# Kernel optimization log

Hardware: AMD Instinct MI355X
Metric: run time of the kernel (lower is better)

Reference implementation:

```python
import jax, jax.numpy as jnp
import numpy as np

B, S1, S2, S3 = 2, 64, 64, 40
INIT_STEP, NUM_CH = 10, 1
WIDTH, MODES, TMODES = 64, 12, 8
GRID_DIM = 3
N_LAYERS = 4


def setup_inputs() -> dict:
    key = jax.random.key(0)
    ks = jax.random.split(key, 16)
    scale = 1.0 / (WIDTH * WIDTH)
    d_in = INIT_STEP * NUM_CH + GRID_DIM
    return {
        "x": jax.random.normal(ks[0], (B, S1, S2, S3, INIT_STEP * NUM_CH), jnp.float32),
        "p_w": jax.random.normal(ks[1], (WIDTH, d_in), jnp.float32) * 0.05,
        "p_b": jnp.zeros((WIDTH,), jnp.float32),
        # radial spectral weights (reflection=False): lower-center column + lower-right block, stacked over 4 layers
        "W_LC": scale * jax.random.uniform(ks[2], (N_LAYERS, WIDTH, WIDTH, MODES, 1, TMODES), jnp.float32),
        "W_LR": scale * jax.random.uniform(ks[3], (N_LAYERS, WIDTH, WIDTH, MODES - 1, MODES - 1, TMODES), jnp.float32),
        "mlp_w1": jax.random.normal(ks[4], (N_LAYERS, WIDTH, WIDTH), jnp.float32) * 0.05,
        "mlp_b1": jnp.zeros((N_LAYERS, WIDTH), jnp.float32),
        "mlp_w2": jax.random.normal(ks[5], (N_LAYERS, WIDTH, WIDTH), jnp.float32) * 0.05,
        "mlp_b2": jnp.zeros((N_LAYERS, WIDTH), jnp.float32),
        "w_w": jax.random.normal(ks[6], (N_LAYERS, WIDTH, WIDTH), jnp.float32) * 0.05,
        "w_b": jnp.zeros((N_LAYERS, WIDTH), jnp.float32),
        "q_w1": jax.random.normal(ks[7], (4 * WIDTH, WIDTH), jnp.float32) * 0.05,
        "q_b1": jnp.zeros((4 * WIDTH,), jnp.float32),
        "q_w2": jax.random.normal(ks[8], (NUM_CH, 4 * WIDTH), jnp.float32) * 0.05,
        "q_b2": jnp.zeros((NUM_CH,), jnp.float32),
    }


def _add_grid(x):
    b, s1, s2, s3, _ = x.shape
    gx = jnp.linspace(0.0, 1.0, s1, dtype=x.dtype)
    gy = jnp.linspace(0.0, 1.0, s2, dtype=x.dtype)
    gt = jnp.linspace(0.0, 1.0, s3, dtype=x.dtype)
    g = jnp.stack(jnp.meshgrid(gx, gy, gt, indexing="ij"), axis=-1)  # (s1,s2,s3,3)
    g = jnp.broadcast_to(g[None], (b, s1, s2, s3, GRID_DIM))
    return jnp.concatenate([x, g], axis=-1)


def _rot90(a):
    # torch.rot90(a, k=1, dims=[-3,-2]) == transpose(flip(a, -2), (-3,-2))
    return jnp.swapaxes(jnp.flip(a, axis=-2), -3, -2)


def _spectral_weights(W_LC, W_LR):
    # W_LC: (i,o,m,1,tm), W_LR: (i,o,m-1,m-1,tm) -> full radial weight (i,o,2m-1,2m-1,tm)
    W_LRf = jnp.concatenate([W_LC[:, :, 1:], W_LR], axis=-2)                    # (i,o,m-1,m,tm)
    W_UR = jnp.concatenate([jnp.flip(W_LC, axis=-3), _rot90(W_LRf)], axis=-2)   # (i,o,m,m,tm)
    W_R = jnp.concatenate([W_UR, W_LRf], axis=-3)                               # (i,o,2m-1,m,tm)
    return jnp.concatenate([jnp.flip(W_R[..., 1:, :], axis=(-3, -2)), W_R], axis=-2)


def _spectral_conv(x, W_LC, W_LR):
    b, ci, s1, s2, s3 = x.shape
    f0y, f0x = s1 // 2, s2 // 2  # index of zero freq after fftshift
    W = _spectral_weights(W_LC, W_LR)
    x_ft = jnp.fft.fftshift(jnp.fft.rfftn(x, axes=(-3, -2, -1)), axes=(-3, -2))
    xs = x_ft[..., f0y - MODES + 1:f0y + MODES, f0x - MODES + 1:f0x + MODES, :TMODES]
    out = jnp.einsum("bixyz,ioxyz->boxyz", xs, W.astype(xs.dtype))
    co = W.shape[1]
    out_ft = jnp.zeros((b, co, s1, s2, s3 // 2 + 1), dtype=xs.dtype)
    out_ft = out_ft.at[..., f0y - MODES + 1:f0y + MODES, f0x - MODES + 1:f0x + MODES, :TMODES].set(out)
    return jnp.fft.irfftn(jnp.fft.ifftshift(out_ft, axes=(-3, -2)), s=(s1, s2, s3), axes=(-3, -2, -1))


def _conv1x1(x, w, b):
    return jnp.einsum("bixyz,oi->boxyz", x, w) + b[None, :, None, None, None]


def _mlp3d(x, w1, b1, w2, b2):
    h = jax.nn.gelu(_conv1x1(x, w1, b1), approximate=False)
    return _conv1x1(h, w2, b2)


def _forward(x, p_w, p_b, W_LC, W_LR, mlp_w1, mlp_b1, mlp_w2, mlp_b2, w_w, w_b, q_w1, q_b1, q_w2, q_b2):
    x = _add_grid(x)
    x = jnp.einsum("bxyzi,wi->bxyzw", x, p_w) + p_b
    x = jnp.transpose(x, (0, 4, 1, 2, 3))  # (B, width, S1, S2, S3)
    for l in range(N_LAYERS):
        x1 = _spectral_conv(x, W_LC[l], W_LR[l])
        x1 = _mlp3d(x1, mlp_w1[l], mlp_b1[l], mlp_w2[l], mlp_b2[l])
        x2 = _conv1x1(x, w_w[l], w_b[l])
        x = x1 + x2
        if l < N_LAYERS - 1:
            x = jax.nn.relu(x)
    x = _mlp3d(x, q_w1, q_b1, q_w2, q_b2)
    return jnp.transpose(x, (0, 2, 3, 4, 1))


def reference(x, p_w, p_b, W_LC, W_LR, mlp_w1, mlp_b1, mlp_w2, mlp_b2, w_w, w_b, q_w1, q_b1, q_w2, q_b2):
    return _forward(x, p_w, p_b, W_LC, W_LR, mlp_w1, mlp_b1, mlp_w2, mlp_b2, w_w, w_b, q_w1, q_b1, q_w2, q_b2)
```

## Files before the change

kernel.cpp:

```cpp
#include <hip/hip_runtime.h>
#include <math.h>

#define PI_D 3.14159265358979323846

__global__ void k_tables(float* tzf, float* tzi, float* tz2, float* tzk,
                         float* txf, float* txi) {
    int t = blockIdx.x * blockDim.x + threadIdx.x;
    if (t < 320) {
        int z = t >> 3, k = t & 7;
        double ang = -2.0 * PI_D * (double)(z * k) / 40.0;
        tzf[t * 2] = (float)cos(ang); tzf[t * 2 + 1] = (float)sin(ang);
        tzi[t * 2] = (float)cos(-ang); tzi[t * 2 + 1] = (float)sin(-ang);
        double s = 1.0 / 163840.0;
        double f = (k == 0) ? s : 2.0 * s;
        tz2[t * 2] = (float)(f * cos(-ang));
        tz2[t * 2 + 1] = (k == 0) ? 0.0f : (float)(-f * sin(-ang));
        tzk[(k * 40 + z) * 2] = (float)cos(ang);
        tzk[(k * 40 + z) * 2 + 1] = (float)sin(ang);
    }
    if (t < 1472) {
        int xx = t / 23, m = t % 23;
        double ang = -2.0 * PI_D * (double)(xx * (m - 11)) / 64.0;
        txf[t * 2] = (float)cos(ang); txf[t * 2 + 1] = (float)sin(ang);
        txi[t * 2] = (float)cos(-ang); txi[t * 2 + 1] = (float)sin(-ang);
    }
}

__global__ void k_wtrans(const float* __restrict__ w2, const float* __restrict__ ww,
                         const float* __restrict__ w1,
                         float* __restrict__ w2t, float* __restrict__ wwt,
                         float* __restrict__ w1t) {
    int gid = blockIdx.x * blockDim.x + threadIdx.x;
    if (gid < 16384) {
        int l = gid >> 12, r = gid & 4095, o = r >> 6, i = r & 63;
        w2t[l * 4096 + i * 64 + o] = w2[l * 4096 + o * 64 + i];
        wwt[l * 4096 + i * 64 + o] = ww[l * 4096 + o * 64 + i];
        w1t[l * 4096 + i * 64 + o] = w1[l * 4096 + o * 64 + i];
    }
}

__global__ void k_lift(const float* __restrict__ xin, const float* __restrict__ pw,
                       const float* __restrict__ pb, float* __restrict__ xo) {
    int gid = blockIdx.x * 256 + threadIdx.x;
    int b = gid / 163840, p = gid % 163840;
    int y = p / 2560, xx = (p / 40) % 64, z = p % 40;
    float v[13];
#pragma unroll
    for (int i = 0; i < 10; i++) v[i] = xin[(size_t)gid * 10 + i];
    v[10] = (float)((double)y / 63.0);
    v[11] = (float)((double)xx / 63.0);
    v[12] = (float)((double)z / 39.0);
    size_t ob = (size_t)b * 10485760 + p;
    for (int c = 0; c < 64; c++) {
        float a = pb[c];
#pragma unroll
        for (int i = 0; i < 13; i++) a += pw[c * 13 + i] * v[i];
        xo[ob + (size_t)c * 163840] = a;
    }
}

__global__ __launch_bounds__(256) void k_fwd_zx(const float* __restrict__ x,
        const float* __restrict__ tzk, const float* __restrict__ txf,
        float* __restrict__ Fx) {
    int bid = blockIdx.x;
    int b = bid >> 12, c = (bid >> 6) & 63, y = bid & 63;
    int t = threadIdx.x;
    __shared__ __align__(16) float xr_[2560];
    __shared__ __align__(16) float tzs[672];
    __shared__ __align__(16) float txs[2944];
    __shared__ __align__(16) float f1[1024];
    const float4* xrow4 = (const float4*)(x + ((size_t)((b * 64 + c) * 4096 + y * 64)) * 40);
    for (int idx = t; idx < 640; idx += 256) ((float4*)xr_)[idx] = xrow4[idx];
    for (int idx = t; idx < 160; idx += 256) {
        int k = idx / 20, q = idx % 20;
        ((float4*)tzs)[k * 21 + q] = ((const float4*)tzk)[idx];
    }
    for (int idx = t; idx < 736; idx += 256) ((float4*)txs)[idx] = ((const float4*)txf)[idx];
    __syncthreads();
    {
        int xx = t >> 3, k = t & 7;
        float sr0 = 0.f, si0 = 0.f, sr1 = 0.f, si1 = 0.f;
        const float2* tzp = (const float2*)(tzs + k * 84);
        const float4* X0 = (const float4*)(xr_ + xx * 40);
        const float4* X1 = (const float4*)(xr_ + (xx + 32) * 40);
        for (int zc = 0; zc < 10; zc++) {
            float4 A = X0[zc], B = X1[zc];
            float2 T0 = tzp[zc * 4], T1v = tzp[zc * 4 + 1];
            float2 T2v = tzp[zc * 4 + 2], T3v = tzp[zc * 4 + 3];
            sr0 = fmaf(A.x, T0.x, sr0);  si0 = fmaf(A.x, T0.y, si0);
            sr0 = fmaf(A.y, T1v.x, sr0); si0 = fmaf(A.y, T1v.y, si0);
            sr0 = fmaf(A.z, T2v.x, sr0); si0 = fmaf(A.z, T2v.y, si0);
            sr0 = fmaf(A.w, T3v.x, sr0); si0 = fmaf(A.w, T3v.y, si0);
            sr1 = fmaf(B.x, T0.x, sr1);  si1 = fmaf(B.x, T0.y, si1);
            sr1 = fmaf(B.y, T1v.x, sr1); si1 = fmaf(B.y, T1v.y, si1);
            sr1 = fmaf(B.z, T2v.x, sr1); si1 = fmaf(B.z, T2v.y, si1);
            sr1 = fmaf(B.w, T3v.x, sr1); si1 = fmaf(B.w, T3v.y, si1);
        }
        ((float2*)f1)[xx * 8 + k] = make_float2(sr0, si0);
        ((float2*)f1)[(xx + 32) * 8 + k] = make_float2(sr1, si1);
    }
    __syncthreads();
    if (t < 184) {
        int m = t >> 3, k = t & 7;
        float sr = 0.f, si = 0.f;
        const float2* f1p = (const float2*)f1;
        const float2* txp = (const float2*)txs;
        for (int xx = 0; xx < 64; xx++) {
            float2 a = f1p[xx * 8 + k];
            float2 w = txp[xx * 23 + m];
            sr = fmaf(a.x, w.x, sr); sr = fmaf(-a.y, w.y, sr);
            si = fmaf(a.x, w.y, si); si = fmaf(a.y, w.x, si);
        }
        size_t g = ((size_t)(((b * 64 + c) * 64 + y) * 23 + m) * 8 + k) * 2;
        Fx[g] = sr; Fx[g + 1] = si;
    }
}

__global__ __launch_bounds__(128) void k_fwd_y(const float* __restrict__ Fx,
        const float* __restrict__ txf, float* __restrict__ Xs) {
    int bid = blockIdx.x;
    int b = bid / 1472, rem = bid % 1472, c = rem / 23, m = rem % 23;
    int t = threadIdx.x;
    __shared__ __align__(16) float s[1024];
    __shared__ __align__(16) float txs[2944];
    for (int idx = t; idx < 512; idx += 128) {
        int y = idx >> 3, k = idx & 7;
        size_t g = ((size_t)(((b * 64 + c) * 64 + y) * 23 + m) * 8 + k);
        ((float2*)s)[idx] = ((const float2*)Fx)[g];
    }
    for (int idx = t; idx < 736; idx += 128) ((float4*)txs)[idx] = ((const float4*)txf)[idx];
    __syncthreads();
    if (t < 92) {
        int n = t >> 2, kp = t & 3;
        float sr0 = 0.f, si0 = 0.f, sr1 = 0.f, si1 = 0.f;
        const float2* txp = (const float2*)txs;
        for (int y = 0; y < 64; y++) {
            float4 S = *(const float4*)&s[y * 16 + kp * 4];
            float2 w = txp[y * 23 + n];
            sr0 = fmaf(S.x, w.x, sr0); sr0 = fmaf(-S.y, w.y, sr0);
            si0 = fmaf(S.x, w.y, si0); si0 = fmaf(S.y, w.x, si0);
            sr1 = fmaf(S.z, w.x, sr1); sr1 = fmaf(-S.w, w.y, sr1);
            si1 = fmaf(S.z, w.y, si1); si1 = fmaf(S.w, w.x, si1);
        }
        size_t g = ((size_t)(((b * 64 + c) * 23 + n) * 23 + m)) * 16 + kp * 4;
        *(float4*)&Xs[g] = make_float4(sr0, si0, sr1, si1);
    }
}

__global__ void k_mix(const float* __restrict__ Xs, const float* __restrict__ WLC,
                      const float* __restrict__ WLR, float* __restrict__ Md) {
    int bid = blockIdx.x;
    int n = bid / 23, m = bid % 23;
    int a = n, c = m, yy, w;
    if (c >= 11) { yy = a; w = c - 11; } else { yy = 22 - a; w = 11 - c; }
    int isLC, idx;
    if (yy >= 12) {
        int p = yy - 12, q = w;
        if (q == 0) { isLC = 1; idx = p + 1; } else { isLC = 0; idx = p * 11 + (q - 1); }
    } else {
        if (w == 0) { isLC = 1; idx = 11 - yy; }
        else {
            int p = w - 1, q = 11 - yy;
            if (q == 0) { isLC = 1; idx = p + 1; } else { isLC = 0; idx = p * 11 + (q - 1); }
        }
    }
    const float* src = isLC ? WLC : WLR;
    int stride = isLC ? 96 : 968;
    int base8 = idx * 8;

    int t = threadIdx.x;
    int o = t >> 3, tt = t & 7;
    __shared__ __align__(16) float wl[8 * 64 * 8];
    __shared__ float xl[256];
    float aR0 = 0.f, aI0 = 0.f, aR1 = 0.f, aI1 = 0.f;
    for (int i0 = 0; i0 < 64; i0 += 8) {
        {
            int il = t >> 6, oo = t & 63;
            const float4* g = (const float4*)(src + (size_t)((i0 + il) * 64 + oo) * stride + base8);
            float4 A = g[0], B = g[1];
            float4* d = (float4*)&wl[(il * 64 + oo) * 8];
            d[0] = A; d[1] = B;
        }
        if (t < 256) {
            int bb = t >> 7, il = (t >> 4) & 7, kk = (t >> 1) & 7, ri = t & 1;
            xl[t] = Xs[((size_t)(((bb * 64 + i0 + il) * 23 + n) * 23 + m) * 8 + kk) * 2 + ri];
        }
        __syncthreads();
#pragma unroll
        for (int il = 0; il < 8; il++) {
            float wv = wl[(il * 64 + o) * 8 + tt];
            float xr0 = xl[(il * 8 + tt) * 2], xi0 = xl[(il * 8 + tt) * 2 + 1];
            float xr1 = xl[128 + (il * 8 + tt) * 2], xi1 = xl[128 + (il * 8 + tt) * 2 + 1];
            aR0 += wv * xr0; aI0 += wv * xi0;
            aR1 += wv * xr1; aI1 += wv * xi1;
        }
        __syncthreads();
    }
    size_t ob0 = ((size_t)((o * 23 + n) * 23 + m) * 8 + tt) * 2;
    size_t ob1 = ((size_t)(((64 + o) * 23 + n) * 23 + m) * 8 + tt) * 2;
    Md[ob0] = aR0; Md[ob0 + 1] = aI0;
    Md[ob1] = aR1; Md[ob1 + 1] = aI1;
}

__global__ __launch_bounds__(256) void k_inv_y(const float* __restrict__ Md,
        const float* __restrict__ txi, float* __restrict__ T1) {
    int bid = blockIdx.x;
    int b = bid / 1472, rem = bid % 1472, o = rem / 23, m = rem % 23;
    int t = threadIdx.x;
    __shared__ __align__(16) float s[368];
    __shared__ __align__(16) float txs[2944];
    if (t < 184) {
        int n = t >> 3, kk = t & 7;
        size_t g = ((size_t)(((b * 64 + o) * 23 + n) * 23 + m) * 8 + kk);
        ((float2*)s)[t] = ((const float2*)Md)[g];
    }
    for (int idx = t; idx < 736; idx += 256) ((float4*)txs)[idx] = ((const float4*)txi)[idx];
    __syncthreads();
    int y = t >> 2, kp = t & 3;
    float sr0 = 0.f, si0 = 0.f, sr1 = 0.f, si1 = 0.f;
    const float2* txp = (const float2*)txs;
    for (int n = 0; n < 23; n++) {
        float4 S = *(const float4*)&s[n * 16 + kp * 4];
        float2 w = txp[y * 23 + n];
        sr0 = fmaf(S.x, w.x, sr0); sr0 = fmaf(-S.y, w.y, sr0);
        si0 = fmaf(S.x, w.y, si0); si0 = fmaf(S.y, w.x, si0);
        sr1 = fmaf(S.z, w.x, sr1); sr1 = fmaf(-S.w, w.y, sr1);
        si1 = fmaf(S.z, w.y, si1); si1 = fmaf(S.w, w.x, si1);
    }
    size_t g = ((size_t)(((b * 64 + o) * 64 + y) * 23 + m)) * 16 + kp * 4;
    *(float4*)&T1[g] = make_float4(sr0, si0, sr1, si1);
}

__global__ __launch_bounds__(256) void k_inv_x(const float* __restrict__ T1,
        const float* __restrict__ txi, float* __restrict__ T2) {
    int bid = blockIdx.x;
    int b = bid >> 12, o = (bid >> 6) & 63, y = bid & 63;
    int t = threadIdx.x;
    __shared__ __align__(16) float s[368];
    __shared__ __align__(16) float txs[2944];
    {
        const float4* src = (const float4*)(T1 + (size_t)((b * 64 + o) * 64 + y) * 368);
        if (t < 92) ((float4*)s)[t] = src[t];
    }
    for (int idx = t; idx < 736; idx += 256) ((float4*)txs)[idx] = ((const float4*)txi)[idx];
    __syncthreads();
    int xx = t >> 2, kp = t & 3;
    float sr0 = 0.f, si0 = 0.f, sr1 = 0.f, si1 = 0.f;
    const float2* txp = (const float2*)txs;
    for (int m = 0; m < 23; m++) {
        float4 S = *(const float4*)&s[m * 16 + kp * 4];
        float2 w = txp[xx * 23 + m];
        sr0 = fmaf(S.x, w.x, sr0); sr0 = fmaf(-S.y, w.y, sr0);
        si0 = fmaf(S.x, w.y, si0); si0 = fmaf(S.y, w.x, si0);
        sr1 = fmaf(S.z, w.x, sr1); sr1 = fmaf(-S.w, w.y, sr1);
        si1 = fmaf(S.z, w.y, si1); si1 = fmaf(S.w, w.x, si1);
    }
    size_t g = ((size_t)((b * 64 + o) * 4096 + y * 64 + xx)) * 16 + kp * 4;
    *(float4*)&T2[g] = make_float4(sr0, si0, sr1, si1);
}

__device__ __forceinline__ float gelu_fast(float x) {
    float u = x * 0.70710678118654752f;
    float a = fabsf(u);
    float t = 1.0f / (1.0f + 0.3275911f * a);
    float poly = t * (0.254829592f + t * (-0.284496736f + t * (1.421413741f +
                 t * (-1.453152027f + t * 1.061405429f))));
    float erfa = 1.0f - poly * __expf(-a * a);
    float er = copysignf(erfa, u);
    return 0.5f * x * (1.0f + er);
}

__global__ __launch_bounds__(256) void k_mlp1(
    const float* __restrict__ t2buf, const float* __restrict__ w1t,
    const float* __restrict__ b1, const float* __restrict__ tz2g,
    float* __restrict__ g) {
    __shared__ __align__(16) float T2s[4096];
    __shared__ __align__(16) float w1ls[4096];
    __shared__ __align__(16) float Hs[4096];
    __shared__ float tzls[640];
    int t = threadIdx.x;
    int site0 = blockIdx.x * 4;
    for (int idx = t; idx < 1024; idx += 256) {
        int sl = idx >> 8, r = idx & 255, i = r >> 2, q = r & 3;
        int site = site0 + sl;
        int b = site >> 12, yx = site & 4095;
        const float4* src = (const float4*)(t2buf + ((size_t)(b * 64 + i) * 4096 + yx) * 16 + q * 4);
        *(float4*)&T2s[sl * 1024 + i * 16 + q * 4] = *src;
    }
    for (int idx = t; idx < 1024; idx += 256)
        *(float4*)&w1ls[idx * 4] = ((const float4*)w1t)[idx];
    for (int idx = t; idx < 640; idx += 256) tzls[idx] = tz2g[idx];
    __syncthreads();
    {
        int sl = t >> 6, u = t & 63;
        int j0 = (u >> 2) * 4, kr0 = (u & 3) * 4;
        float c0 = 0.f, c1 = 0.f, c2 = 0.f, c3 = 0.f, c4 = 0.f, c5 = 0.f, c6 = 0.f, c7 = 0.f;
        float c8 = 0.f, c9 = 0.f, c10 = 0.f, c11 = 0.f, c12 = 0.f, c13 = 0.f, c14 = 0.f, c15 = 0.f;
        int tb = sl * 1024 + kr0;
        for (int i = 0; i < 64; i++) {
            float4 W = *(const float4*)&w1ls[i * 64 + j0];
            float4 T = *(const float4*)&T2s[tb + i * 16];
            c0  = fmaf(W.x, T.x, c0);  c1  = fmaf(W.x, T.y, c1);
            c2  = fmaf(W.x, T.z, c2);  c3  = fmaf(W.x, T.w, c3);
            c4  = fmaf(W.y, T.x, c4);  c5  = fmaf(W.y, T.y, c5);
            c6  = fmaf(W.y, T.z, c6);  c7  = fmaf(W.y, T.w, c7);
            c8  = fmaf(W.z, T.x, c8);  c9  = fmaf(W.z, T.y, c9);
            c10 = fmaf(W.z, T.z, c10); c11 = fmaf(W.z, T.w, c11);
            c12 = fmaf(W.w, T.x, c12); c13 = fmaf(W.w, T.y, c13);
            c14 = fmaf(W.w, T.z, c14); c15 = fmaf(W.w, T.w, c15);
        }
        int hb = sl * 1024 + j0 * 16 + kr0;
        *(float4*)&Hs[hb]      = make_float4(c0, c1, c2, c3);
        *(float4*)&Hs[hb + 16] = make_float4(c4, c5, c6, c7);
        *(float4*)&Hs[hb + 32] = make_float4(c8, c9, c10, c11);
        *(float4*)&Hs[hb + 48] = make_float4(c12, c13, c14, c15);
    }
    __syncthreads();
    {
        int sl = t >> 6, j = t & 63;
        int site = site0 + sl;
        int b = site >> 12, yx = site & 4095;
        int hb = sl * 1024 + j * 16;
        float4 H0 = *(const float4*)&Hs[hb];
        float4 H1 = *(const float4*)&Hs[hb + 4];
        float4 H2 = *(const float4*)&Hs[hb + 8];
        float4 H3 = *(const float4*)&Hs[hb + 12];
        float b1j = b1[j];
        size_t obase = (size_t)j * 327680 + (size_t)b * 163840 + yx * 40;
        for (int zc = 0; zc < 10; zc++) {
            float4 outv;
#pragma unroll
            for (int zi = 0; zi < 4; zi++) {
                int z = zc * 4 + zi;
                const float4* tz = (const float4*)&tzls[z * 16];
                float4 T0 = tz[0], T1v = tz[1], T2v = tz[2], T3 = tz[3];
                float v = H0.x * T0.x;
                v = fmaf(H0.y, T0.y, v); v = fmaf(H0.z, T0.z, v); v = fmaf(H0.w, T0.w, v);
                v = fmaf(H1.x, T1v.x, v); v = fmaf(H1.y, T1v.y, v);
                v = fmaf(H1.z, T1v.z, v); v = fmaf(H1.w, T1v.w, v);
                v = fmaf(H2.x, T2v.x, v); v = fmaf(H2.y, T2v.y, v);
                v = fmaf(H2.z, T2v.z, v); v = fmaf(H2.w, T2v.w, v);
                v = fmaf(H3.x, T3.x, v); v = fmaf(H3.y, T3.y, v);
                v = fmaf(H3.z, T3.z, v); v = fmaf(H3.w, T3.w, v);
                float h = b1j + v;
                float gv = gelu_fast(h);
                if (zi == 0) outv.x = gv; else if (zi == 1) outv.y = gv;
                else if (zi == 2) outv.z = gv; else outv.w = gv;
            }
            *(float4*)&g[obase + zc * 4] = outv;
        }
    }
}

#define FMAR8(R, Wc) \
    a##R##0 = fmaf(Wc, X0.x, a##R##0); a##R##1 = fmaf(Wc, X0.y, a##R##1); \
    a##R##2 = fmaf(Wc, X0.z, a##R##2); a##R##3 = fmaf(Wc, X0.w, a##R##3); \
    a##R##4 = fmaf(Wc, X1.x, a##R##4); a##R##5 = fmaf(Wc, X1.y, a##R##5); \
    a##R##6 = fmaf(Wc, X1.z, a##R##6); a##R##7 = fmaf(Wc, X1.w, a##R##7);

__global__ __launch_bounds__(256) void k_mlp2(
    const float* __restrict__ g, float* __restrict__ x,
    const float* __restrict__ w2t, const float* __restrict__ b2,
    const float* __restrict__ wwt, const float* __restrict__ wb, int dorelu) {
    __shared__ __align__(16) float wls[4096];
    int t = threadIdx.x;
    int P0 = blockIdx.x * 256;
    int b = P0 / 163840, pl = P0 % 163840;
    size_t xbase = (size_t)b * 10485760 + pl;
    int o0 = (t >> 5) * 8, p0 = (t & 31) * 8;
#define INITR(R) float a##R##0 = b2[o0 + R] + wb[o0 + R]; \
    float a##R##1 = a##R##0, a##R##2 = a##R##0, a##R##3 = a##R##0, \
          a##R##4 = a##R##0, a##R##5 = a##R##0, a##R##6 = a##R##0, a##R##7 = a##R##0;
    INITR(0) INITR(1) INITR(2) INITR(3) INITR(4) INITR(5) INITR(6) INITR(7)
#undef INITR
    for (int idx = t; idx < 1024; idx += 256)
        ((float4*)wls)[idx] = ((const float4*)wwt)[idx];
    __syncthreads();
    for (int i = 0; i < 64; i++) {
        const float4* wp = (const float4*)&wls[i * 64 + o0];
        float4 W0 = wp[0], W1 = wp[1];
        const float* xp = x + xbase + (size_t)i * 163840 + p0;
        float4 X0 = *(const float4*)xp, X1 = *(const float4*)(xp + 4);
        FMAR8(0, W0.x) FMAR8(1, W0.y) FMAR8(2, W0.z) FMAR8(3, W0.w)
        FMAR8(4, W1.x) FMAR8(5, W1.y) FMAR8(6, W1.z) FMAR8(7, W1.w)
    }
    __syncthreads();
    for (int idx = t; idx < 1024; idx += 256)
        ((float4*)wls)[idx] = ((const float4*)w2t)[idx];
    __syncthreads();
    for (int j = 0; j < 64; j++) {
        const float4* wp = (const float4*)&wls[j * 64 + o0];
        float4 W0 = wp[0], W1 = wp[1];
        const float* gp = g + (size_t)j * 327680 + P0 + p0;
        float4 X0 = *(const float4*)gp, X1 = *(const float4*)(gp + 4);
        FMAR8(0, W0.x) FMAR8(1, W0.y) FMAR8(2, W0.z) FMAR8(3, W0.w)
        FMAR8(4, W1.x) FMAR8(5, W1.y) FMAR8(6, W1.z) FMAR8(7, W1.w)
    }
#define STROW(R) { \
        float4 R0, R1; \
        if (dorelu) { \
            R0 = make_float4(fmaxf(a##R##0, 0.f), fmaxf(a##R##1, 0.f), fmaxf(a##R##2, 0.f), fmaxf(a##R##3, 0.f)); \
            R1 = make_float4(fmaxf(a##R##4, 0.f), fmaxf(a##R##5, 0.f), fmaxf(a##R##6, 0.f), fmaxf(a##R##7, 0.f)); \
        } else { \
            R0 = make_float4(a##R##0, a##R##1, a##R##2, a##R##3); \
            R1 = make_float4(a##R##4, a##R##5, a##R##6, a##R##7); \
        } \
        float* op = x + xbase + (size_t)(o0 + R) * 163840 + p0; \
        *(float4*)op = R0; *(float4*)(op + 4) = R1; }
    STROW(0) STROW(1) STROW(2) STROW(3) STROW(4) STROW(5) STROW(6) STROW(7)
#undef STROW
}

__global__ __launch_bounds__(256, 4) void k_head(
    const float* __restrict__ xcur,
    const float* __restrict__ qw1, const float* __restrict__ qb1,
    const float* __restrict__ qw2, const float* __restrict__ qb2,
    float* __restrict__ outp) {
    int t = threadIdx.x;
    int P0 = blockIdx.x * 256;
    int b = P0 / 163840, pl = P0 % 163840;
    size_t base = (size_t)b * 10485760 + pl + t;
    float xr[64];
#pragma unroll
    for (int i = 0; i < 64; i++) xr[i] = xcur[base + (size_t)i * 163840];
    float acc = qb2[0];
    for (int j = 0; j < 256; j++) {
        const float4* wrow = (const float4*)(qw1 + (size_t)j * 64);
        float p[4] = {0.f, 0.f, 0.f, 0.f};
#pragma unroll
        for (int q = 0; q < 16; ++q) {
            float4 W = wrow[q];
            float s = p[q & 3];
            s = fmaf(W.x, xr[4 * q + 0], s);
            s = fmaf(W.y, xr[4 * q + 1], s);
            s = fmaf(W.z, xr[4 * q + 2], s);
            s = fmaf(W.w, xr[4 * q + 3], s);
            p[q & 3] = s;
        }
        float h = qb1[j] + ((p[0] + p[1]) + (p[2] + p[3]));
        acc = fmaf(qw2[j], gelu_fast(h), acc);
    }
    outp[P0 + t] = acc;
}

extern "C" void kernel_launch(void* const* d_in, const int* in_sizes, int n_in,
                              void* d_out, int out_size, void* d_ws, size_t ws_size,
                              hipStream_t stream) {
    const float* x_in = (const float*)d_in[0];
    const float* p_w  = (const float*)d_in[1];
    const float* p_b  = (const float*)d_in[2];
    const float* W_LC = (const float*)d_in[3];
    const float* W_LR = (const float*)d_in[4];
    const float* m_w1 = (const float*)d_in[5];
    const float* m_b1 = (const float*)d_in[6];
    const float* m_w2 = (const float*)d_in[7];
    const float* m_b2 = (const float*)d_in[8];
    const float* w_w  = (const float*)d_in[9];
    const float* w_b  = (const float*)d_in[10];
    const float* q_w1 = (const float*)d_in[11];
    const float* q_b1 = (const float*)d_in[12];
    const float* q_w2 = (const float*)d_in[13];
    const float* q_b2 = (const float*)d_in[14];

    char* ws = (char*)d_ws;
    float* tzf = (float*)(ws + 0);
    float* tzi = (float*)(ws + 2560);
    float* tz2 = (float*)(ws + 5120);
    float* tzk = (float*)(ws + 7680);
    float* txf = (float*)(ws + 10240);
    float* txi = (float*)(ws + 22016);
    float* w2t = (float*)(ws + 65536);
    float* wwt = (float*)(ws + 131072);
    float* w1t = (float*)(ws + 196608);
    size_t off = 262144;
    float* xA = (float*)(ws + off); off += 83886080ull;
    float* gbuf = (float*)(ws + off); off += 83886080ull;
    float* Fx = (float*)(ws + off); off += 12058624ull;
    float* Xs = (float*)(ws + off); off += 4333568ull;
    float* Md = (float*)(ws + off); off += 4333568ull;
    float* T1 = (float*)(ws + off); off += 12058624ull;
    float* T2 = (float*)(ws + off); off += 33554432ull;

    k_tables<<<6, 256, 0, stream>>>(tzf, tzi, tz2, tzk, txf, txi);
    k_wtrans<<<64, 256, 0, stream>>>(m_w2, w_w, m_w1, w2t, wwt, w1t);
    k_lift<<<1280, 256, 0, stream>>>(x_in, p_w, p_b, xA);

    for (int l = 0; l < 4; l++) {
        k_fwd_zx<<<8192, 256, 0, stream>>>(xA, tzk, txf, Fx);
        k_fwd_y<<<2944, 128, 0, stream>>>(Fx, txf, Xs);
        k_mix<<<529, 512, 0, stream>>>(Xs, W_LC + (size_t)l * 393216,
                                       W_LR + (size_t)l * 3964928, Md);
        k_inv_y<<<2944, 256, 0, stream>>>(Md, txi, T1);
        k_inv_x<<<8192, 256, 0, stream>>>(T1, txi, T2);
        k_mlp1<<<2048, 256, 0, stream>>>(T2, w1t + (size_t)l * 4096, m_b1 + l * 64,
                                         tz2, gbuf);
        k_mlp2<<<1280, 256, 0, stream>>>(gbuf, xA, w2t + (size_t)l * 4096, m_b2 + l * 64,
                                         wwt + (size_t)l * 4096, w_b + l * 64,
                                         (l < 3) ? 1 : 0);
    }
    k_head<<<1280, 256, 0, stream>>>(xA, q_w1, q_b1, q_w2, q_b2, (float*)d_out);
}
```

Baseline: 1.353 ms.

## Restructure projection head as register-tiled 8x8 GEMM with LDS weights

The head kernel previously had each thread hold 64 channels of one point and loop over 256 hidden units, reading weights from global memory through scalar loads. It now transposes q_w1 once, stages 64-hidden-unit slabs of it in LDS, and computes an 8-output by 8-point register tile per thread with float4 loads. GELU and the q_w2 dot are applied in the epilogue, and partial sums are then reduced across output groups through shared memory. This raises arithmetic intensity and drops redundant weight traffic. In exchange the activation rows are re-read from global memory four times, and there are extra barriers.

```diff
diff --git a/kernel.cpp b/kernel.cpp
--- a/kernel.cpp
+++ b/kernel.cpp
@@ -27,15 +27,17 @@
 }
 
 __global__ void k_wtrans(const float* __restrict__ w2, const float* __restrict__ ww,
-                         const float* __restrict__ w1,
+                         const float* __restrict__ w1, const float* __restrict__ qw1,
                          float* __restrict__ w2t, float* __restrict__ wwt,
-                         float* __restrict__ w1t) {
+                         float* __restrict__ w1t, float* __restrict__ q1t) {
     int gid = blockIdx.x * blockDim.x + threadIdx.x;
     if (gid < 16384) {
         int l = gid >> 12, r = gid & 4095, o = r >> 6, i = r & 63;
         w2t[l * 4096 + i * 64 + o] = w2[l * 4096 + o * 64 + i];
         wwt[l * 4096 + i * 64 + o] = ww[l * 4096 + o * 64 + i];
         w1t[l * 4096 + i * 64 + o] = w1[l * 4096 + o * 64 + i];
+        int j = gid >> 6, iq = gid & 63;
+        q1t[iq * 256 + j] = qw1[gid];
     }
 }
 
@@ -411,36 +413,69 @@
 #undef STROW
 }
 
-__global__ __launch_bounds__(256, 4) void k_head(
-    const float* __restrict__ xcur,
-    const float* __restrict__ qw1, const float* __restrict__ qb1,
-    const float* __restrict__ qw2, const float* __restrict__ qb2,
-    float* __restrict__ outp) {
+__global__ __launch_bounds__(256) void k_head(
+    const float* __restrict__ xcur, const float* __restrict__ q1t,
+    const float* __restrict__ qb1, const float* __restrict__ qw2,
+    const float* __restrict__ qb2, float* __restrict__ outp) {
+    __shared__ __align__(16) float wls[4096];
     int t = threadIdx.x;
     int P0 = blockIdx.x * 256;
     int b = P0 / 163840, pl = P0 % 163840;
-    size_t base = (size_t)b * 10485760 + pl + t;
-    float xr[64];
+    size_t xbase = (size_t)b * 10485760 + pl;
+    int o0 = (t >> 5) * 8, p0 = (t & 31) * 8;
+    float outa0 = 0.f, outa1 = 0.f, outa2 = 0.f, outa3 = 0.f;
+    float outa4 = 0.f, outa5 = 0.f, outa6 = 0.f, outa7 = 0.f;
+    for (int c = 0; c < 4; c++) {
+        if (c) __syncthreads();
+        for (int idx = t; idx < 1024; idx += 256) {
+            int i = idx >> 4, q = idx & 15;
+            ((float4*)wls)[i * 16 + q] = *(const float4*)&q1t[i * 256 + c * 64 + q * 4];
+        }
+        __syncthreads();
+        float a00 = 0.f, a01 = 0.f, a02 = 0.f, a03 = 0.f, a04 = 0.f, a05 = 0.f, a06 = 0.f, a07 = 0.f;
+        float a10 = 0.f, a11 = 0.f, a12 = 0.f, a13 = 0.f, a14 = 0.f, a15 = 0.f, a16 = 0.f, a17 = 0.f;
+        float a20 = 0.f, a21 = 0.f, a22 = 0.f, a23 = 0.f, a24 = 0.f, a25 = 0.f, a26 = 0.f, a27 = 0.f;
+        float a30 = 0.f, a31 = 0.f, a32 = 0.f, a33 = 0.f, a34 = 0.f, a35 = 0.f, a36 = 0.f, a37 = 0.f;
+        float a40 = 0.f, a41 = 0.f, a42 = 0.f, a43 = 0.f, a44 = 0.f, a45 = 0.f, a46 = 0.f, a47 = 0.f;
+        float a50 = 0.f, a51 = 0.f, a52 = 0.f, a53 = 0.f, a54 = 0.f, a55 = 0.f, a56 = 0.f, a57 = 0.f;
+        float a60 = 0.f, a61 = 0.f, a62 = 0.f, a63 = 0.f, a64 = 0.f, a65 = 0.f, a66 = 0.f, a67 = 0.f;
+        float a70 = 0.f, a71 = 0.f, a72 = 0.f, a73 = 0.f, a74 = 0.f, a75 = 0.f, a76 = 0.f, a77 = 0.f;
+        for (int i = 0; i < 64; i++) {
+            const float4* wp = (const float4*)&wls[i * 64 + o0];
+            float4 W0 = wp[0], W1 = wp[1];
+            const float* xp = xcur + xbase + (size_t)i * 163840 + p0;
+            float4 X0 = *(const float4*)xp, X1 = *(const float4*)(xp + 4);
+            FMAR8(0, W0.x) FMAR8(1, W0.y) FMAR8(2, W0.z) FMAR8(3, W0.w)
+            FMAR8(4, W1.x) FMAR8(5, W1.y) FMAR8(6, W1.z) FMAR8(7, W1.w)
+        }
+        int jb = c * 64 + o0;
+#define EPIR(R) { float bj = qb1[jb + R]; float wj = qw2[jb + R]; \
+        outa0 = fmaf(wj, gelu_fast(a##R##0 + bj), outa0); \
+        outa1 = fmaf(wj, gelu_fast(a##R##1 + bj), outa1); \
+        outa2 = fmaf(wj, gelu_fast(a##R##2 + bj), outa2); \
+        outa3 = fmaf(wj, gelu_fast(a##R##3 + bj), outa3); \
+        outa4 = fmaf(wj, gelu_fast(a##R##4 + bj), outa4); \
+        outa5 = fmaf(wj, gelu_fast(a##R##5 + bj), outa5); \
+        outa6 = fmaf(wj, gelu_fast(a##R##6 + bj), outa6); \
+        outa7 = fmaf(wj, gelu_fast(a##R##7 + bj), outa7); }
+        EPIR(0) EPIR(1) EPIR(2) EPIR(3) EPIR(4) EPIR(5) EPIR(6) EPIR(7)
+#undef EPIR
+    }
+    __syncthreads();
+    {
+        int og = t >> 5;
+        float* rl = wls;
+        *(float4*)&rl[og * 272 + p0]     = make_float4(outa0, outa1, outa2, outa3);
+        *(float4*)&rl[og * 272 + p0 + 4] = make_float4(outa4, outa5, outa6, outa7);
+    }
+    __syncthreads();
+    {
+        const float* rl = wls;
+        float s = qb2[0];
 #pragma unroll
-    for (int i = 0; i < 64; i++) xr[i] = xcur[base + (size_t)i * 163840];
-    float acc = qb2[0];
-    for (int j = 0; j < 256; j++) {
-        const float4* wrow = (const float4*)(qw1 + (size_t)j * 64);
-        float p[4] = {0.f, 0.f, 0.f, 0.f};
-#pragma unroll
-        for (int q = 0; q < 16; ++q) {
-            float4 W = wrow[q];
-            float s = p[q & 3];
-            s = fmaf(W.x, xr[4 * q + 0], s);
-            s = fmaf(W.y, xr[4 * q + 1], s);
-            s = fmaf(W.z, xr[4 * q + 2], s);
-            s = fmaf(W.w, xr[4 * q + 3], s);
-            p[q & 3] = s;
-        }
-        float h = qb1[j] + ((p[0] + p[1]) + (p[2] + p[3]));
-        acc = fmaf(qw2[j], gelu_fast(h), acc);
-    }
-    outp[P0 + t] = acc;
+        for (int g2 = 0; g2 < 8; g2++) s += rl[g2 * 272 + t];
+        outp[P0 + t] = s;
+    }
 }
 
 extern "C" void kernel_launch(void* const* d_in, const int* in_sizes, int n_in,
@@ -472,7 +507,8 @@
     float* w2t = (float*)(ws + 65536);
     float* wwt = (float*)(ws + 131072);
     float* w1t = (float*)(ws + 196608);
-    size_t off = 262144;
+    float* q1t = (float*)(ws + 262144);
+    size_t off = 327680;
     float* xA = (float*)(ws + off); off += 83886080ull;
     float* gbuf = (float*)(ws + off); off += 83886080ull;
     float* Fx = (float*)(ws + off); off += 12058624ull;
@@ -482,7 +518,7 @@
     float* T2 = (float*)(ws + off); off += 33554432ull;
 
     k_tables<<<6, 256, 0, stream>>>(tzf, tzi, tz2, tzk, txf, txi);
-    k_wtrans<<<64, 256, 0, stream>>>(m_w2, w_w, m_w1, w2t, wwt, w1t);
+    k_wtrans<<<64, 256, 0, stream>>>(m_w2, w_w, m_w1, q_w1, w2t, wwt, w1t, q1t);
     k_lift<<<1280, 256, 0, stream>>>(x_in, p_w, p_b, xA);
 
     for (int l = 0; l < 4; l++) {
@@ -498,5 +534,5 @@
                                          wwt + (size_t)l * 4096, w_b + l * 64,
                                          (l < 3) ? 1 : 0);
     }
-    k_head<<<1280, 256, 0, stream>>>(xA, q_w1, q_b1, q_w2, q_b2, (float*)d_out);
-}
+    k_head<<<1280, 256, 0, stream>>>(xA, q1t, q_b1, q_w2, q_b2, (float*)d_out);
+}
```

New measurement: 1.341 ms. About the same (-0.9%).
